# Kernel tuning notes

Measured on AMD Instinct MI355X. Metric: run time of the kernel, lower is better.

## Reference

```python
import jax, jax.numpy as jnp
import numpy as np

N_NODES = 50000
N_EDGES = 1000000


def _gat_layer(x, edge_index, edge_prob, W, Wt, a_src, a_trg, a_tp, b, Wskip, concat):
    """One GATLayerImp3 forward (eval mode, dropout=identity).
    x: [N,Fin], edge_index: [2,E] (row0=src,row1=trg), edge_prob: [E,1].
    a_*: [1,H,F]. Returns [N,H*F] if concat else [N,F]."""
    N = x.shape[0]
    H, F = a_src.shape[1], a_src.shape[2]
    src, trg = edge_index[0], edge_index[1]

    proj = (x @ W).reshape(N, H, F)                      # [N,H,F]
    tp_proj = (edge_prob @ Wt).reshape(-1, H, F)         # [E,H,F]

    s_src = jnp.sum(proj * a_src, axis=-1)               # [N,H]
    s_trg = jnp.sum(proj * a_trg, axis=-1)               # [N,H]
    s_tp = jnp.sum(tp_proj * a_tp, axis=-1)              # [E,H]

    scores = jax.nn.leaky_relu(s_src[src] + s_trg[trg] + s_tp, 0.2)  # [E,H]
    exp_s = jnp.exp(scores - jnp.max(scores))            # global max, as in original
    denom = jax.ops.segment_sum(exp_s, trg, num_segments=N)[trg]     # [E,H]
    att = (exp_s / (denom + 1e-16))[:, :, None]          # [E,H,1]

    out = jax.ops.segment_sum(proj[src] * att, trg, num_segments=N)  # [N,H,F]

    if Wskip is None:  # dims match -> identity skip
        out = out + x[:, None, :]
    else:
        out = out + (x @ Wskip).reshape(N, H, F)

    out = out.reshape(N, H * F) if concat else out.mean(axis=1)
    return jax.nn.elu(out + b)


def setup_inputs() -> dict:
    key = jax.random.key(0)
    ks = jax.random.split(key, 16)
    s = 0.05
    return {
        "x": jax.random.normal(ks[0], (N_NODES, 128), jnp.float32),
        "edge_index": jax.random.randint(ks[1], (2, N_EDGES), 0, N_NODES, jnp.int32),
        "edge_prob": jax.random.uniform(ks[2], (N_EDGES, 1), jnp.float32),
        "W1": jax.random.normal(ks[3], (128, 128), jnp.float32) * s,
        "Wt1": jax.random.normal(ks[4], (1, 128), jnp.float32) * s,
        "a_src1": jax.random.normal(ks[5], (1, 8, 16), jnp.float32) * s,
        "a_trg1": jax.random.normal(ks[6], (1, 8, 16), jnp.float32) * s,
        "a_tp1": jax.random.normal(ks[7], (1, 8, 16), jnp.float32) * s,
        "b1": jnp.zeros((128,), jnp.float32),
        "Wskip1": jax.random.normal(ks[8], (128, 128), jnp.float32) * s,
        "W2": jax.random.normal(ks[9], (128, 128), jnp.float32) * s,
        "Wt2": jax.random.normal(ks[10], (1, 128), jnp.float32) * s,
        "a_src2": jax.random.normal(ks[11], (1, 1, 128), jnp.float32) * s,
        "a_trg2": jax.random.normal(ks[12], (1, 1, 128), jnp.float32) * s,
        "a_tp2": jax.random.normal(ks[13], (1, 1, 128), jnp.float32) * s,
        "b2": jnp.zeros((128,), jnp.float32),
    }


def reference(x, edge_index, edge_prob, W1, Wt1, a_src1, a_trg1, a_tp1, b1, Wskip1,
              W2, Wt2, a_src2, a_trg2, a_tp2, b2):
    h = _gat_layer(x, edge_index, edge_prob, W1, Wt1, a_src1, a_trg1, a_tp1, b1,
                   Wskip1, concat=True)                    # [N, 128]
    out = _gat_layer(h, edge_index, edge_prob, W2, Wt2, a_src2, a_trg2, a_tp2, b2,
                     None, concat=False)                   # [N, 128]
    return out
```

## Files before the change

kernel.cpp:

```cpp
#include <hip/hip_runtime.h>
#include <hip/hip_fp16.h>
#include <cstdint>
#include <cstddef>

__global__ __launch_bounds__(256) void gemm128_f32(const float* __restrict__ A,
                                                   const float* __restrict__ B,
                                                   float* __restrict__ C,
                                                   __half* __restrict__ Ch, int M) {
  __shared__ float Ast[32][68];
  __shared__ float Bs[32][132];
  const int t = threadIdx.x;
  const int row0 = blockIdx.x * 64;
  const int ty = t >> 4, tx = t & 15;

  float acc[4][8] = {};

  for (int kt = 0; kt < 4; ++kt) {
#pragma unroll
    for (int i = 0; i < 2; ++i) {
      int idx = t + i * 256;
      int r = idx >> 3;
      int kq = (idx & 7) * 4;
      float4 v = make_float4(0.f, 0.f, 0.f, 0.f);
      if (row0 + r < M)
        v = *reinterpret_cast<const float4*>(A + (size_t)(row0 + r) * 128 + kt * 32 + kq);
      Ast[kq + 0][r] = v.x;
      Ast[kq + 1][r] = v.y;
      Ast[kq + 2][r] = v.z;
      Ast[kq + 3][r] = v.w;
    }
#pragma unroll
    for (int i = 0; i < 4; ++i) {
      int idx = t + i * 256;
      int k = idx >> 5;
      int c4 = (idx & 31) * 4;
      *reinterpret_cast<float4*>(&Bs[k][c4]) =
          *reinterpret_cast<const float4*>(B + (size_t)(kt * 32 + k) * 128 + c4);
    }
    __syncthreads();

#pragma unroll
    for (int k = 0; k < 32; ++k) {
      float4 a4 = *reinterpret_cast<float4*>(&Ast[k][ty * 4]);
      float4 b0 = *reinterpret_cast<float4*>(&Bs[k][tx * 4]);
      float4 b1 = *reinterpret_cast<float4*>(&Bs[k][64 + tx * 4]);
      float a[4] = {a4.x, a4.y, a4.z, a4.w};
      float b[8] = {b0.x, b0.y, b0.z, b0.w, b1.x, b1.y, b1.z, b1.w};
#pragma unroll
      for (int i = 0; i < 4; ++i)
#pragma unroll
        for (int j = 0; j < 8; ++j) acc[i][j] += a[i] * b[j];
    }
    __syncthreads();
  }

#pragma unroll
  for (int i = 0; i < 4; ++i) {
    int r = row0 + ty * 4 + i;
    if (r < M) {
      float4 lo = make_float4(acc[i][0], acc[i][1], acc[i][2], acc[i][3]);
      float4 hi = make_float4(acc[i][4], acc[i][5], acc[i][6], acc[i][7]);
      *reinterpret_cast<float4*>(C + (size_t)r * 128 + tx * 4) = lo;
      *reinterpret_cast<float4*>(C + (size_t)r * 128 + 64 + tx * 4) = hi;
      if (Ch) {
        __half2* hp0 = reinterpret_cast<__half2*>(Ch + (size_t)r * 128 + tx * 4);
        __half2* hp1 = reinterpret_cast<__half2*>(Ch + (size_t)r * 128 + 64 + tx * 4);
        hp0[0] = __floats2half2_rn(lo.x, lo.y);
        hp0[1] = __floats2half2_rn(lo.z, lo.w);
        hp1[0] = __floats2half2_rn(hi.x, hi.y);
        hp1[1] = __floats2half2_rn(hi.z, hi.w);
      }
    }
  }
}

__global__ void count_deg(const int* __restrict__ trg, int* __restrict__ deg, int E) {
  int e = blockIdx.x * blockDim.x + threadIdx.x;
  if (e < E) atomicAdd(&deg[trg[e]], 1);
}

__global__ void scan_bsum(const int* __restrict__ deg, int* __restrict__ bsum, int N) {
  __shared__ int ws[4];
  int i = blockIdx.x * 256 + threadIdx.x;
  int v = (i < N) ? deg[i] : 0;
#pragma unroll
  for (int off = 1; off < 64; off <<= 1) v += __shfl_xor(v, off);
  if ((threadIdx.x & 63) == 0) ws[threadIdx.x >> 6] = v;
  __syncthreads();
  if (threadIdx.x == 0) bsum[blockIdx.x] = ws[0] + ws[1] + ws[2] + ws[3];
}

__global__ void scan_top(const int* __restrict__ bsum, int* __restrict__ boff,
                         int* __restrict__ row_off, int nb, int N) {
  __shared__ int s[256];
  int t = threadIdx.x;
  int v = (t < nb) ? bsum[t] : 0;
  s[t] = v;
  __syncthreads();
#pragma unroll
  for (int off = 1; off < 256; off <<= 1) {
    int x = s[t];
    int add = (t >= off) ? s[t - off] : 0;
    __syncthreads();
    s[t] = x + add;
    __syncthreads();
  }
  if (t < nb) boff[t] = (t == 0) ? 0 : s[t - 1];
  if (t == 0) row_off[N] = s[255];
}

__global__ void scan_local(const int* __restrict__ deg, const int* __restrict__ boff,
                           int* __restrict__ row_off, int N) {
  __shared__ int s[256];
  int t = threadIdx.x;
  int i = blockIdx.x * 256 + t;
  int v = (i < N) ? deg[i] : 0;
  s[t] = v;
  __syncthreads();
#pragma unroll
  for (int off = 1; off < 256; off <<= 1) {
    int x = s[t];
    int add = (t >= off) ? s[t - off] : 0;
    __syncthreads();
    s[t] = x + add;
    __syncthreads();
  }
  if (i < N) row_off[i] = boff[blockIdx.x] + (t == 0 ? 0 : s[t - 1]);
}

__global__ __launch_bounds__(256) void bucket_scatter(
    const int* __restrict__ src, const int* __restrict__ trg,
    const float* __restrict__ ep, const int* __restrict__ row_off,
    int* __restrict__ bcur, int2* __restrict__ staging, int E, int N) {
  __shared__ int cnt[256], boff[256], rowb[256];
  const int nb2 = (N + 255) >> 8;
  if (threadIdx.x < nb2) cnt[threadIdx.x] = 0;
  __syncthreads();
  const int base = blockIdx.x * 1024;
  int b_[4], r_[4], s_[4], p_[4];
#pragma unroll
  for (int j = 0; j < 4; ++j) {
    int e = base + threadIdx.x + j * 256;
    bool v = e < E;
    int tg = v ? trg[e] : 0;
    int sc = v ? src[e] : 0;
    p_[j] = v ? __float_as_int(ep[e]) : 0;
    b_[j] = tg >> 8;
    s_[j] = sc | ((tg & 255) << 16);
    r_[j] = v ? atomicAdd(&cnt[b_[j]], 1) : -1;
  }
  __syncthreads();
  if (threadIdx.x < nb2) {
    int c = cnt[threadIdx.x];
    boff[threadIdx.x] = c ? atomicAdd(&bcur[threadIdx.x], c) : 0;
    rowb[threadIdx.x] = row_off[threadIdx.x << 8];
  }
  __syncthreads();
#pragma unroll
  for (int j = 0; j < 4; ++j) {
    if (r_[j] >= 0) {
      int b = b_[j];
      staging[(size_t)rowb[b] + boff[b] + r_[j]] = make_int2(s_[j], p_[j]);
    }
  }
}

__global__ __launch_bounds__(256) void bucket_place(
    const int2* __restrict__ staging, const int* __restrict__ row_off,
    int2* __restrict__ edge2, int N) {
  __shared__ int cur[256];
  __shared__ int rbase[256];
  const int n0 = blockIdx.x << 8;
  const int nn = min(256, N - n0);
  if (threadIdx.x < nn) {
    cur[threadIdx.x] = 0;
    rbase[threadIdx.x] = row_off[n0 + threadIdx.x];
  }
  __syncthreads();
  const int lo = row_off[n0];
  const int hi = row_off[min(n0 + 256, N)];
  for (int i = lo + threadIdx.x; i < hi; i += 256) {
    int2 v = staging[i];
    int ln = (v.x >> 16) & 255;
    int pos = rbase[ln] + atomicAdd(&cur[ln], 1);
    edge2[pos] = make_int2(v.x & 0xFFFF, v.y);
  }
}

template <int H, int F>
__global__ void node_scores(const float* __restrict__ proj, const float* __restrict__ a_src,
                            const float* __restrict__ a_trg, float* __restrict__ ssrc,
                            float* __restrict__ strg, int N) {
  int idx = blockIdx.x * blockDim.x + threadIdx.x;
  if (idx >= N * H) return;
  int n = idx / H, h = idx % H;
  const float* p = proj + (size_t)n * (H * F) + h * F;
  const float* as = a_src + h * F;
  const float* at = a_trg + h * F;
  float d1 = 0.f, d2 = 0.f;
#pragma unroll
  for (int f = 0; f < F; f += 4) {
    float4 pv = *reinterpret_cast<const float4*>(p + f);
    float4 av = *reinterpret_cast<const float4*>(as + f);
    float4 tv = *reinterpret_cast<const float4*>(at + f);
    d1 += pv.x * av.x + pv.y * av.y + pv.z * av.z + pv.w * av.w;
    d2 += pv.x * tv.x + pv.y * tv.y + pv.z * tv.z + pv.w * tv.w;
  }
  ssrc[idx] = d1;
  strg[idx] = d2;
}

template <int H, int F>
__global__ void aggregate(const int2* __restrict__ edge2, const int* __restrict__ row_off,
                          const float* __restrict__ ssrc, const float* __restrict__ strg,
                          const float* __restrict__ Wt, const float* __restrict__ a_tp,
                          const __half* __restrict__ projh, const float* __restrict__ skip,
                          const float* __restrict__ bias, float* __restrict__ out, int N) {
  int wid = (blockIdx.x * blockDim.x + threadIdx.x) >> 6;
  if (wid >= N) return;
  const int lane = threadIdx.x & 63;
  const int half = lane >> 5;
  const int fl = (lane & 31) * 4;
  const int h = fl / F;

  float4 wt4 = *reinterpret_cast<const float4*>(Wt + fl);
  float4 at4 = *reinterpret_cast<const float4*>(a_tp + fl);
  float ch = wt4.x * at4.x + wt4.y * at4.y + wt4.z * at4.z + wt4.w * at4.w;
#pragma unroll
  for (int off = 1; off < (F / 4); off <<= 1) ch += __shfl_xor(ch, off);

  const float mt = strg[(size_t)wid * H + h];
  const int beg = row_off[wid];
  const int end = row_off[wid + 1];

  float ax = 0.f, ay = 0.f, az = 0.f, aw = 0.f;
  float denom = 0.f;

  for (int i = beg; i < end; i += 8) {
    int   s[4];
    float pe[4], vd[4];
    float2 raw[4];
#pragma unroll
    for (int q = 0; q < 4; ++q) {
      int ii = i + q * 2 + half;
      bool v = ii < end;
      int2 e2 = v ? edge2[ii] : make_int2(0, 0);
      s[q] = e2.x;
      pe[q] = __int_as_float(e2.y);
      vd[q] = v ? 1.f : 0.f;
    }
#pragma unroll
    for (int q = 0; q < 4; ++q)
      raw[q] = *reinterpret_cast<const float2*>(projh + (size_t)s[q] * (H * F) + fl);
#pragma unroll
    for (int q = 0; q < 4; ++q) {
      float sc = ssrc[(size_t)s[q] * H + h] + mt + pe[q] * ch;
      sc = sc > 0.f ? sc : 0.2f * sc;
      float ee = __expf(sc) * vd[q];
      __half2 h01 = *reinterpret_cast<__half2*>(&raw[q].x);
      __half2 h23 = *reinterpret_cast<__half2*>(&raw[q].y);
      float2 f01 = __half22float2(h01);
      float2 f23 = __half22float2(h23);
      denom += ee;
      ax += f01.x * ee;
      ay += f01.y * ee;
      az += f23.x * ee;
      aw += f23.y * ee;
    }
  }

  denom += __shfl_xor(denom, 32);
  ax += __shfl_xor(ax, 32);
  ay += __shfl_xor(ay, 32);
  az += __shfl_xor(az, 32);
  aw += __shfl_xor(aw, 32);

  if (half == 0) {
    float inv = 1.0f / (denom + 1e-16f);
    size_t base = (size_t)wid * (H * F) + fl;
    float4 sk = *reinterpret_cast<const float4*>(skip + base);
    float4 bi = *reinterpret_cast<const float4*>(bias + fl);
    float o0 = ax * inv + sk.x + bi.x;
    float o1 = ay * inv + sk.y + bi.y;
    float o2 = az * inv + sk.z + bi.z;
    float o3 = aw * inv + sk.w + bi.w;
    o0 = o0 > 0.f ? o0 : __expf(o0) - 1.f;
    o1 = o1 > 0.f ? o1 : __expf(o1) - 1.f;
    o2 = o2 > 0.f ? o2 : __expf(o2) - 1.f;
    o3 = o3 > 0.f ? o3 : __expf(o3) - 1.f;
    float4 ov = make_float4(o0, o1, o2, o3);
    *reinterpret_cast<float4*>(out + base) = ov;
  }
}

extern "C" void kernel_launch(void* const* d_in, const int* in_sizes, int n_in,
                              void* d_out, int out_size, void* d_ws, size_t ws_size,
                              hipStream_t stream) {
  const float* x      = (const float*)d_in[0];
  const int*   ei     = (const int*)  d_in[1];
  const float* ep     = (const float*)d_in[2];
  const float* W1     = (const float*)d_in[3];
  const float* Wt1    = (const float*)d_in[4];
  const float* a_src1 = (const float*)d_in[5];
  const float* a_trg1 = (const float*)d_in[6];
  const float* a_tp1  = (const float*)d_in[7];
  const float* b1     = (const float*)d_in[8];
  const float* Wskip1 = (const float*)d_in[9];
  const float* W2     = (const float*)d_in[10];
  const float* Wt2    = (const float*)d_in[11];
  const float* a_src2 = (const float*)d_in[12];
  const float* a_trg2 = (const float*)d_in[13];
  const float* a_tp2  = (const float*)d_in[14];
  const float* b2     = (const float*)d_in[15];

  const int N = in_sizes[0] / 128;
  const int E = in_sizes[1] / 2;
  const int* srcA = ei;
  const int* trgA = ei + E;

  char* ws = (char*)d_ws;
  size_t off = 0;
  auto alloc = [&](size_t bytes) {
    void* p = ws + off;
    off += (bytes + 255) & ~(size_t)255;
    return p;
  };
  int*    deg     = (int*)   alloc((size_t)(N + 256) * 4);
  int*    bcur    = deg + N;
  int*    row_off = (int*)   alloc((size_t)(N + 1) * 4);
  int*    bsum    = (int*)   alloc((size_t)256 * 4);
  int*    boff    = (int*)   alloc((size_t)256 * 4);
  int2*   staging = (int2*)  alloc((size_t)E * 8);
  int2*   edge2   = (int2*)  alloc((size_t)E * 8);
  float*  proj    = (float*) alloc((size_t)N * 128 * 4);
  __half* projh   = (__half*)alloc((size_t)N * 128 * 2);
  float*  skip1   = (float*) alloc((size_t)N * 128 * 4);
  float*  hbuf    = (float*) alloc((size_t)N * 128 * 4);
  float*  ssrc    = (float*) alloc((size_t)N * 8 * 4);
  float*  strg    = (float*) alloc((size_t)N * 8 * 4);
  (void)ws_size; (void)n_in; (void)out_size;

  hipMemsetAsync(deg, 0, (size_t)(N + 256) * 4, stream);

  const int eb = (E + 255) / 256;
  const int gb = (N + 63) / 64;
  const int nb = (N + 255) / 256;

  count_deg<<<eb, 256, 0, stream>>>(trgA, deg, E);
  scan_bsum<<<nb, 256, 0, stream>>>(deg, bsum, N);
  scan_top<<<1, 256, 0, stream>>>(bsum, boff, row_off, nb, N);
  scan_local<<<nb, 256, 0, stream>>>(deg, boff, row_off, N);
  bucket_scatter<<<(E + 1023) / 1024, 256, 0, stream>>>(srcA, trgA, ep, row_off, bcur,
                                                        staging, E, N);
  bucket_place<<<nb, 256, 0, stream>>>(staging, row_off, edge2, N);

  gemm128_f32<<<gb, 256, 0, stream>>>(x, W1, proj, projh, N);
  gemm128_f32<<<gb, 256, 0, stream>>>(x, Wskip1, skip1, (__half*)nullptr, N);
  node_scores<8, 16><<<(N * 8 + 255) / 256, 256, 0, stream>>>(proj, a_src1, a_trg1, ssrc, strg, N);
  aggregate<8, 16><<<(N + 3) / 4, 256, 0, stream>>>(edge2, row_off, ssrc, strg, Wt1, a_tp1,
                                                    projh, skip1, b1, hbuf, N);

  gemm128_f32<<<gb, 256, 0, stream>>>(hbuf, W2, proj, projh, N);
  node_scores<1, 128><<<(N + 255) / 256, 256, 0, stream>>>(proj, a_src2, a_trg2, ssrc, strg, N);
  aggregate<1, 128><<<(N + 3) / 4, 256, 0, stream>>>(edge2, row_off, ssrc, strg, Wt2, a_tp2,
                                                     projh, hbuf, b2, (float*)d_out, N);
}
```

Measured before the change: 407.3 us.

## Build CSR from coarse bucket histogram and fuse the two layer-1 GEMMs

Replaces the per-node degree count and three-pass scan with a block-local histogram over 256-node buckets and a single small scan. Per-node row offsets are now computed inside bucket_place with a local shared-memory scan. The W1 and Wskip1 GEMMs are merged into one kernel that reads x once, which doubles accumulator registers and shared memory per block. Index arithmetic in aggregate is narrowed to 32-bit shifts, relying on H*F==128 and on offsets fitting in int.

```diff
diff --git a/kernel.cpp b/kernel.cpp
--- a/kernel.cpp
+++ b/kernel.cpp
@@ -2,6 +2,91 @@
 #include <hip/hip_fp16.h>
 #include <cstdint>
 #include <cstddef>
+
+__global__ __launch_bounds__(256) void gemm_dual(const float* __restrict__ A,
+                                                 const float* __restrict__ B1,
+                                                 const float* __restrict__ B2,
+                                                 float* __restrict__ C1,
+                                                 __half* __restrict__ Ch1,
+                                                 float* __restrict__ C2, int M) {
+  __shared__ float Ast[32][68];
+  __shared__ float Bs1[32][132];
+  __shared__ float Bs2[32][132];
+  const int t = threadIdx.x;
+  const int row0 = blockIdx.x * 64;
+  const int ty = t >> 4, tx = t & 15;
+
+  float acc1[4][8] = {};
+  float acc2[4][8] = {};
+
+  for (int kt = 0; kt < 4; ++kt) {
+#pragma unroll
+    for (int i = 0; i < 2; ++i) {
+      int idx = t + i * 256;
+      int r = idx >> 3;
+      int kq = (idx & 7) * 4;
+      float4 v = make_float4(0.f, 0.f, 0.f, 0.f);
+      if (row0 + r < M)
+        v = *reinterpret_cast<const float4*>(A + (size_t)(row0 + r) * 128 + kt * 32 + kq);
+      Ast[kq + 0][r] = v.x;
+      Ast[kq + 1][r] = v.y;
+      Ast[kq + 2][r] = v.z;
+      Ast[kq + 3][r] = v.w;
+    }
+#pragma unroll
+    for (int i = 0; i < 4; ++i) {
+      int idx = t + i * 256;
+      int k = idx >> 5;
+      int c4 = (idx & 31) * 4;
+      *reinterpret_cast<float4*>(&Bs1[k][c4]) =
+          *reinterpret_cast<const float4*>(B1 + (size_t)(kt * 32 + k) * 128 + c4);
+      *reinterpret_cast<float4*>(&Bs2[k][c4]) =
+          *reinterpret_cast<const float4*>(B2 + (size_t)(kt * 32 + k) * 128 + c4);
+    }
+    __syncthreads();
+
+#pragma unroll
+    for (int k = 0; k < 32; ++k) {
+      float4 a4 = *reinterpret_cast<float4*>(&Ast[k][ty * 4]);
+      float a[4] = {a4.x, a4.y, a4.z, a4.w};
+      float4 p0 = *reinterpret_cast<float4*>(&Bs1[k][tx * 4]);
+      float4 p1 = *reinterpret_cast<float4*>(&Bs1[k][64 + tx * 4]);
+      float b1v[8] = {p0.x, p0.y, p0.z, p0.w, p1.x, p1.y, p1.z, p1.w};
+      float4 q0 = *reinterpret_cast<float4*>(&Bs2[k][tx * 4]);
+      float4 q1 = *reinterpret_cast<float4*>(&Bs2[k][64 + tx * 4]);
+      float b2v[8] = {q0.x, q0.y, q0.z, q0.w, q1.x, q1.y, q1.z, q1.w};
+#pragma unroll
+      for (int i = 0; i < 4; ++i)
+#pragma unroll
+        for (int j = 0; j < 8; ++j) {
+          acc1[i][j] += a[i] * b1v[j];
+          acc2[i][j] += a[i] * b2v[j];
+        }
+    }
+    __syncthreads();
+  }
+
+#pragma unroll
+  for (int i = 0; i < 4; ++i) {
+    int r = row0 + ty * 4 + i;
+    if (r < M) {
+      float4 lo = make_float4(acc1[i][0], acc1[i][1], acc1[i][2], acc1[i][3]);
+      float4 hi = make_float4(acc1[i][4], acc1[i][5], acc1[i][6], acc1[i][7]);
+      *reinterpret_cast<float4*>(C1 + (size_t)r * 128 + tx * 4) = lo;
+      *reinterpret_cast<float4*>(C1 + (size_t)r * 128 + 64 + tx * 4) = hi;
+      __half2* hp0 = reinterpret_cast<__half2*>(Ch1 + (size_t)r * 128 + tx * 4);
+      __half2* hp1 = reinterpret_cast<__half2*>(Ch1 + (size_t)r * 128 + 64 + tx * 4);
+      hp0[0] = __floats2half2_rn(lo.x, lo.y);
+      hp0[1] = __floats2half2_rn(lo.z, lo.w);
+      hp1[0] = __floats2half2_rn(hi.x, hi.y);
+      hp1[1] = __floats2half2_rn(hi.z, hi.w);
+      float4 lo2 = make_float4(acc2[i][0], acc2[i][1], acc2[i][2], acc2[i][3]);
+      float4 hi2 = make_float4(acc2[i][4], acc2[i][5], acc2[i][6], acc2[i][7]);
+      *reinterpret_cast<float4*>(C2 + (size_t)r * 128 + tx * 4) = lo2;
+      *reinterpret_cast<float4*>(C2 + (size_t)r * 128 + 64 + tx * 4) = hi2;
+    }
+  }
+}
 
 __global__ __launch_bounds__(256) void gemm128_f32(const float* __restrict__ A,
                                                    const float* __restrict__ B,
@@ -74,27 +159,28 @@
   }
 }
 
-__global__ void count_deg(const int* __restrict__ trg, int* __restrict__ deg, int E) {
-  int e = blockIdx.x * blockDim.x + threadIdx.x;
-  if (e < E) atomicAdd(&deg[trg[e]], 1);
-}
-
-__global__ void scan_bsum(const int* __restrict__ deg, int* __restrict__ bsum, int N) {
-  __shared__ int ws[4];
-  int i = blockIdx.x * 256 + threadIdx.x;
-  int v = (i < N) ? deg[i] : 0;
-#pragma unroll
-  for (int off = 1; off < 64; off <<= 1) v += __shfl_xor(v, off);
-  if ((threadIdx.x & 63) == 0) ws[threadIdx.x >> 6] = v;
-  __syncthreads();
-  if (threadIdx.x == 0) bsum[blockIdx.x] = ws[0] + ws[1] + ws[2] + ws[3];
-}
-
-__global__ void scan_top(const int* __restrict__ bsum, int* __restrict__ boff,
-                         int* __restrict__ row_off, int nb, int N) {
+__global__ __launch_bounds__(256) void bucket_hist(const int* __restrict__ trg,
+                                                   int* __restrict__ bhist, int E) {
+  __shared__ int cnt[256];
+  cnt[threadIdx.x] = 0;
+  __syncthreads();
+  const int base = blockIdx.x * 1024;
+#pragma unroll
+  for (int j = 0; j < 4; ++j) {
+    int e = base + threadIdx.x + j * 256;
+    if (e < E) atomicAdd(&cnt[trg[e] >> 8], 1);
+  }
+  __syncthreads();
+  int c = cnt[threadIdx.x];
+  if (c) atomicAdd(&bhist[threadIdx.x], c);
+}
+
+__global__ void scan196(const int* __restrict__ bhist, int* __restrict__ boffx,
+                        int* __restrict__ bcur, int* __restrict__ row_off, int nb, int N) {
   __shared__ int s[256];
   int t = threadIdx.x;
-  int v = (t < nb) ? bsum[t] : 0;
+  bcur[t] = 0;
+  int v = (t < nb) ? bhist[t] : 0;
   s[t] = v;
   __syncthreads();
 #pragma unroll
@@ -105,32 +191,16 @@
     s[t] = x + add;
     __syncthreads();
   }
-  if (t < nb) boff[t] = (t == 0) ? 0 : s[t - 1];
-  if (t == 0) row_off[N] = s[255];
-}
-
-__global__ void scan_local(const int* __restrict__ deg, const int* __restrict__ boff,
-                           int* __restrict__ row_off, int N) {
-  __shared__ int s[256];
-  int t = threadIdx.x;
-  int i = blockIdx.x * 256 + t;
-  int v = (i < N) ? deg[i] : 0;
-  s[t] = v;
-  __syncthreads();
-#pragma unroll
-  for (int off = 1; off < 256; off <<= 1) {
-    int x = s[t];
-    int add = (t >= off) ? s[t - off] : 0;
-    __syncthreads();
-    s[t] = x + add;
-    __syncthreads();
-  }
-  if (i < N) row_off[i] = boff[blockIdx.x] + (t == 0 ? 0 : s[t - 1]);
+  if (t < nb) boffx[t] = (t == 0) ? 0 : s[t - 1];
+  if (t == 0) {
+    boffx[nb] = s[255];
+    row_off[N] = s[255];
+  }
 }
 
 __global__ __launch_bounds__(256) void bucket_scatter(
     const int* __restrict__ src, const int* __restrict__ trg,
-    const float* __restrict__ ep, const int* __restrict__ row_off,
+    const float* __restrict__ ep, const int* __restrict__ boffx,
     int* __restrict__ bcur, int2* __restrict__ staging, int E, int N) {
   __shared__ int cnt[256], boff[256], rowb[256];
   const int nb2 = (N + 255) >> 8;
@@ -153,36 +223,51 @@
   if (threadIdx.x < nb2) {
     int c = cnt[threadIdx.x];
     boff[threadIdx.x] = c ? atomicAdd(&bcur[threadIdx.x], c) : 0;
-    rowb[threadIdx.x] = row_off[threadIdx.x << 8];
+    rowb[threadIdx.x] = boffx[threadIdx.x];
   }
   __syncthreads();
 #pragma unroll
   for (int j = 0; j < 4; ++j) {
     if (r_[j] >= 0) {
       int b = b_[j];
-      staging[(size_t)rowb[b] + boff[b] + r_[j]] = make_int2(s_[j], p_[j]);
+      staging[rowb[b] + boff[b] + r_[j]] = make_int2(s_[j], p_[j]);
     }
   }
 }
 
 __global__ __launch_bounds__(256) void bucket_place(
-    const int2* __restrict__ staging, const int* __restrict__ row_off,
-    int2* __restrict__ edge2, int N) {
-  __shared__ int cur[256];
-  __shared__ int rbase[256];
+    const int2* __restrict__ staging, const int* __restrict__ boffx,
+    int* __restrict__ row_off, int2* __restrict__ edge2, int N) {
+  __shared__ int cnt[256], loc[256], cur[256];
+  const int t = threadIdx.x;
   const int n0 = blockIdx.x << 8;
   const int nn = min(256, N - n0);
-  if (threadIdx.x < nn) {
-    cur[threadIdx.x] = 0;
-    rbase[threadIdx.x] = row_off[n0 + threadIdx.x];
-  }
-  __syncthreads();
-  const int lo = row_off[n0];
-  const int hi = row_off[min(n0 + 256, N)];
-  for (int i = lo + threadIdx.x; i < hi; i += 256) {
+  cnt[t] = 0;
+  __syncthreads();
+  const int lo = boffx[blockIdx.x];
+  const int hi = boffx[blockIdx.x + 1];
+  for (int i = lo + t; i < hi; i += 256) {
+    atomicAdd(&cnt[(staging[i].x >> 16) & 255], 1);
+  }
+  __syncthreads();
+  loc[t] = cnt[t];
+  __syncthreads();
+#pragma unroll
+  for (int off = 1; off < 256; off <<= 1) {
+    int x = loc[t];
+    int add = (t >= off) ? loc[t - off] : 0;
+    __syncthreads();
+    loc[t] = x + add;
+    __syncthreads();
+  }
+  int excl = loc[t] - cnt[t];
+  if (t < nn) row_off[n0 + t] = lo + excl;
+  cur[t] = lo + excl;
+  __syncthreads();
+  for (int i = lo + t; i < hi; i += 256) {
     int2 v = staging[i];
     int ln = (v.x >> 16) & 255;
-    int pos = rbase[ln] + atomicAdd(&cur[ln], 1);
+    int pos = atomicAdd(&cur[ln], 1);
     edge2[pos] = make_int2(v.x & 0xFFFF, v.y);
   }
 }
@@ -216,6 +301,7 @@
                           const float* __restrict__ Wt, const float* __restrict__ a_tp,
                           const __half* __restrict__ projh, const float* __restrict__ skip,
                           const float* __restrict__ bias, float* __restrict__ out, int N) {
+  static_assert(H * F == 128, "offset shift assumes H*F==128");
   int wid = (blockIdx.x * blockDim.x + threadIdx.x) >> 6;
   if (wid >= N) return;
   const int lane = threadIdx.x & 63;
@@ -229,7 +315,7 @@
 #pragma unroll
   for (int off = 1; off < (F / 4); off <<= 1) ch += __shfl_xor(ch, off);
 
-  const float mt = strg[(size_t)wid * H + h];
+  const float mt = strg[wid * H + h];
   const int beg = row_off[wid];
   const int end = row_off[wid + 1];
 
@@ -251,10 +337,10 @@
     }
 #pragma unroll
     for (int q = 0; q < 4; ++q)
-      raw[q] = *reinterpret_cast<const float2*>(projh + (size_t)s[q] * (H * F) + fl);
+      raw[q] = *reinterpret_cast<const float2*>(projh + (s[q] << 7) + fl);
 #pragma unroll
     for (int q = 0; q < 4; ++q) {
-      float sc = ssrc[(size_t)s[q] * H + h] + mt + pe[q] * ch;
+      float sc = ssrc[s[q] * H + h] + mt + pe[q] * ch;
       sc = sc > 0.f ? sc : 0.2f * sc;
       float ee = __expf(sc) * vd[q];
       __half2 h01 = *reinterpret_cast<__half2*>(&raw[q].x);
@@ -277,7 +363,7 @@
 
   if (half == 0) {
     float inv = 1.0f / (denom + 1e-16f);
-    size_t base = (size_t)wid * (H * F) + fl;
+    int base = (wid << 7) + fl;
     float4 sk = *reinterpret_cast<const float4*>(skip + base);
     float4 bi = *reinterpret_cast<const float4*>(bias + fl);
     float o0 = ax * inv + sk.x + bi.x;
@@ -325,11 +411,10 @@
     off += (bytes + 255) & ~(size_t)255;
     return p;
   };
-  int*    deg     = (int*)   alloc((size_t)(N + 256) * 4);
-  int*    bcur    = deg + N;
+  int*    bhist   = (int*)   alloc((size_t)256 * 4);
+  int*    bcur    = (int*)   alloc((size_t)256 * 4);
+  int*    boffx   = (int*)   alloc((size_t)257 * 4);
   int*    row_off = (int*)   alloc((size_t)(N + 1) * 4);
-  int*    bsum    = (int*)   alloc((size_t)256 * 4);
-  int*    boff    = (int*)   alloc((size_t)256 * 4);
   int2*   staging = (int2*)  alloc((size_t)E * 8);
   int2*   edge2   = (int2*)  alloc((size_t)E * 8);
   float*  proj    = (float*) alloc((size_t)N * 128 * 4);
@@ -340,22 +425,18 @@
   float*  strg    = (float*) alloc((size_t)N * 8 * 4);
   (void)ws_size; (void)n_in; (void)out_size;
 
-  hipMemsetAsync(deg, 0, (size_t)(N + 256) * 4, stream);
-
-  const int eb = (E + 255) / 256;
+  hipMemsetAsync(bhist, 0, 256 * 4, stream);
+
+  const int eb4 = (E + 1023) / 1024;
   const int gb = (N + 63) / 64;
   const int nb = (N + 255) / 256;
 
-  count_deg<<<eb, 256, 0, stream>>>(trgA, deg, E);
-  scan_bsum<<<nb, 256, 0, stream>>>(deg, bsum, N);
-  scan_top<<<1, 256, 0, stream>>>(bsum, boff, row_off, nb, N);
-  scan_local<<<nb, 256, 0, stream>>>(deg, boff, row_off, N);
-  bucket_scatter<<<(E + 1023) / 1024, 256, 0, stream>>>(srcA, trgA, ep, row_off, bcur,
-                                                        staging, E, N);
-  bucket_place<<<nb, 256, 0, stream>>>(staging, row_off, edge2, N);
-
-  gemm128_f32<<<gb, 256, 0, stream>>>(x, W1, proj, projh, N);
-  gemm128_f32<<<gb, 256, 0, stream>>>(x, Wskip1, skip1, (__half*)nullptr, N);
+  bucket_hist<<<eb4, 256, 0, stream>>>(trgA, bhist, E);
+  scan196<<<1, 256, 0, stream>>>(bhist, boffx, bcur, row_off, nb, N);
+  bucket_scatter<<<eb4, 256, 0, stream>>>(srcA, trgA, ep, boffx, bcur, staging, E, N);
+  bucket_place<<<nb, 256, 0, stream>>>(staging, boffx, row_off, edge2, N);
+
+  gemm_dual<<<gb, 256, 0, stream>>>(x, W1, Wskip1, proj, projh, skip1, N);
   node_scores<8, 16><<<(N * 8 + 255) / 256, 256, 0, stream>>>(proj, a_src1, a_trg1, ssrc, strg, N);
   aggregate<8, 16><<<(N + 3) / 4, 256, 0, stream>>>(edge2, row_off, ssrc, strg, Wt1, a_tp1,
                                                     projh, skip1, b1, hbuf, N);
```

Result: no change. 405.4 us (-0.5%).
